# Optimization experiments

Hardware: AMD Instinct MI355X
Metric: run time of the kernel (lower is better)

## Reference

```python
import jax, jax.numpy as jnp
import numpy as np

N = 100000   # nodes
E = 1600000  # edges (avg degree 16)
G = 1024     # graphs in batch
F = 128      # node feature dim
H = 128      # hidden channels


def setup_inputs() -> dict:
    key = jax.random.key(0)
    ks = jax.random.split(key, 12)
    s = 1.0 / np.sqrt(H)
    x = jax.random.normal(ks[0], (N, F), dtype=jnp.float32)
    edge_index = jax.random.randint(ks[1], (2, E), 0, N, dtype=jnp.int32)
    batch = jnp.sort(jax.random.randint(ks[2], (N,), 0, G, dtype=jnp.int32))
    return {
        "x": x,
        "edge_index": edge_index,
        "batch": batch,
        "W1": jax.random.normal(ks[3], (F, H), dtype=jnp.float32) * s,
        "b1": jnp.zeros((H,), jnp.float32),
        "W2": jax.random.normal(ks[4], (H, H), dtype=jnp.float32) * s,
        "b2": jnp.zeros((H,), jnp.float32),
        "W3": jax.random.normal(ks[5], (H, H), dtype=jnp.float32) * s,
        "b3": jnp.zeros((H,), jnp.float32),
        "W4": jax.random.normal(ks[6], (H, H), dtype=jnp.float32) * s,
        "b4": jnp.zeros((H,), jnp.float32),
        "linW": jax.random.normal(ks[7], (H, 2), dtype=jnp.float32) * s,
        "linb": jnp.zeros((2,), jnp.float32),
    }


def _gcn_conv(h, W, b, src, dst, norm, n):
    # h' = D^{-1/2}(A+I)D^{-1/2} (h W) + b   (PyG GCNConv default)
    m = h @ W                              # [n, H]
    msg = m[src] * norm[:, None]           # [E+n, H] gather + scale
    out = jax.ops.segment_sum(msg, dst, num_segments=n)
    return out + b


def reference(x, edge_index, batch, W1, b1, W2, b2, W3, b3, W4, b4, linW, linb):
    n = x.shape[0]
    loops = jnp.arange(n, dtype=edge_index.dtype)
    src = jnp.concatenate([edge_index[0], loops])   # add self-loops
    dst = jnp.concatenate([edge_index[1], loops])
    deg = jax.ops.segment_sum(jnp.ones_like(dst, dtype=x.dtype), dst, num_segments=n)
    dinv = jax.lax.rsqrt(deg)                       # deg >= 1 due to self-loops
    norm = dinv[src] * dinv[dst]                    # [E+n]

    h = jax.nn.relu(_gcn_conv(x, W1, b1, src, dst, norm, n))
    h = jax.nn.relu(_gcn_conv(h, W2, b2, src, dst, norm, n))
    h = jax.nn.relu(_gcn_conv(h, W3, b3, src, dst, norm, n))
    h = jax.nn.relu(_gcn_conv(h, W4, b4, src, dst, norm, n))

    # global_mean_pool over `batch` segment ids
    counts = jax.ops.segment_sum(jnp.ones((n,), x.dtype), batch, num_segments=G)
    pooled = jax.ops.segment_sum(h, batch, num_segments=G) / jnp.maximum(counts, 1.0)[:, None]

    # dropout p=0.5 is identity in eval mode
    return pooled @ linW + linb
```

## Files before the change

### kernel.cpp

```cpp
#include <hip/hip_runtime.h>
#include <math.h>

#define NF 128
#define NU 64
#define NQ 32
#define TROWS 32
#define ARS 68
#define CRS 132
#define QS  16.0f
#define QIS 0.0625f

#define SRC_BITS 18
#define SRC_MASK ((1u << SRC_BITS) - 1u)
#define BCS 32
#define EPB 4096

typedef unsigned int  u32;
typedef unsigned short u16;
typedef u32 b4 __attribute__((ext_vector_type(2)));
typedef short bf16x8 __attribute__((ext_vector_type(8)));
typedef float f32x4 __attribute__((ext_vector_type(4)));
typedef float f32x2 __attribute__((ext_vector_type(2)));

__device__ inline u16 f2bf(float f) {
    u32 u = __float_as_uint(f);
    return (u16)((u + 0x7fffu + ((u >> 16) & 1u)) >> 16);
}
__device__ inline u32 pack2(float a, float b) {
    return (u32)f2bf(a) | ((u32)f2bf(b) << 16);
}
__device__ inline float bflo(u32 u) { return __uint_as_float(u << 16); }
__device__ inline float bfhi(u32 u) { return __uint_as_float(u & 0xffff0000u); }

__device__ inline u32 pack4(float a, float b, float c, float d) {
    u32 v = __builtin_amdgcn_cvt_pk_fp8_f32(a, b, 0, false);
    v = __builtin_amdgcn_cvt_pk_fp8_f32(c, d, v, true);
    return v;
}
__device__ inline void acc4(float4& a, u32 q) {
    f32x2 lo = __builtin_amdgcn_cvt_pk_f32_fp8(q, false);
    f32x2 hi = __builtin_amdgcn_cvt_pk_f32_fp8(q, true);
    a.x += lo[0]; a.y += lo[1]; a.z += hi[0]; a.w += hi[1];
}


__global__ __launch_bounds__(256) void k_bcnt(const int* __restrict__ ei,
                                              int* bcnt, int E, int bshift) {
    __shared__ int h[256];
    int t = threadIdx.x;
    h[t] = 0;
    __syncthreads();
    int base = blockIdx.x * EPB;
    #pragma unroll
    for (int k = 0; k < EPB / 256; ++k) {
        int e = base + k * 256 + t;
        if (e < E) atomicAdd(&h[ei[E + e] >> bshift], 1);
    }
    __syncthreads();
    if (h[t]) atomicAdd(&bcnt[t * BCS], h[t]);
}

__global__ __launch_bounds__(256) void k_bscan(const int* __restrict__ bcnt,
                                               int* bbase, int* bcur) {
    __shared__ int s[256];
    int t = threadIdx.x;
    int v = bcnt[t * BCS];
    s[t] = v;
    for (int d = 1; d < 256; d <<= 1) {
        __syncthreads();
        int a = (t >= d) ? s[t - d] : 0;
        __syncthreads();
        s[t] += a;
    }
    __syncthreads();
    bbase[t + 1] = s[t];
    bcur[t * BCS] = s[t] - v;
    if (t == 0) bbase[0] = 0;
}

__global__ __launch_bounds__(256) void k_bscat(const int* __restrict__ ei,
                                               int* bcur, u32* __restrict__ pairs,
                                               int E, int bshift) {
    __shared__ int h[256];
    __shared__ int rb[256];
    int t = threadIdx.x;
    h[t] = 0;
    __syncthreads();
    int base = blockIdx.x * EPB;
    #pragma unroll
    for (int k = 0; k < EPB / 256; ++k) {
        int e = base + k * 256 + t;
        if (e < E) atomicAdd(&h[ei[E + e] >> bshift], 1);
    }
    __syncthreads();
    int c = h[t];
    if (c) rb[t] = atomicAdd(&bcur[t * BCS], c);
    h[t] = 0;
    __syncthreads();
    #pragma unroll
    for (int k = 0; k < EPB / 256; ++k) {
        int e = base + k * 256 + t;
        if (e < E) {
            int d = ei[E + e];
            int b = d >> bshift;
            int p = rb[b] + atomicAdd(&h[b], 1);
            u32 rel = (u32)(d - (b << bshift));
            pairs[p] = (rel << SRC_BITS) | (u32)ei[e];
        }
    }
}

__global__ __launch_bounds__(256) void k_ndeg(const u32* __restrict__ pairs,
                                              const int* __restrict__ bbase,
                                              int* __restrict__ cnt, int n, int bshift) {
    extern __shared__ int sh[];
    int b = blockIdx.x;
    int bsz = 1 << bshift;
    int b0 = b << bshift;
    int t = threadIdx.x;
    for (int i = t; i < bsz; i += 256) sh[i] = 0;
    __syncthreads();
    int lo = bbase[b], hi = bbase[b + 1];
    for (int j = lo + t; j < hi; j += 256)
        atomicAdd(&sh[pairs[j] >> SRC_BITS], 1);
    __syncthreads();
    for (int i = t; i < bsz; i += 256) {
        int node = b0 + i;
        if (node < n) cnt[node] = sh[i];
    }
}

__global__ void k_scan1(const int* __restrict__ cnt, float* dinv,
                        int* offs, int* bsum, int n) {
    __shared__ int s[256];
    int t = threadIdx.x;
    int i = blockIdx.x * 256 + t;
    int v = 0;
    if (i < n) {
        int real = cnt[i] + 1;
        dinv[i] = 1.0f / sqrtf((float)real);
        v = (real + 3) & ~3;
    }
    s[t] = v;
    for (int d = 1; d < 256; d <<= 1) {
        __syncthreads();
        int add = (t >= d) ? s[t - d] : 0;
        __syncthreads();
        s[t] += add;
    }
    __syncthreads();
    if (i <= n) offs[i] = s[t] - v;
    if (t == 255) bsum[blockIdx.x] = s[255];
}

__global__ void k_scan2(int* bsum, int nb) {
    __shared__ int s[512];
    int t = threadIdx.x;
    int v = (t < nb) ? bsum[t] : 0;
    s[t] = v;
    for (int d = 1; d < 512; d <<= 1) {
        __syncthreads();
        int add = (t >= d) ? s[t - d] : 0;
        __syncthreads();
        s[t] += add;
    }
    __syncthreads();
    if (t < nb) bsum[t] = s[t] - v;
}

__global__ void k_scan3(int* offs, const int* __restrict__ bsum, int n) {
    int i = blockIdx.x * 256 + threadIdx.x;
    if (i <= n) offs[i] += bsum[blockIdx.x];
}

__global__ __launch_bounds__(256) void k_csr(const u32* __restrict__ pairs,
                                             const int* __restrict__ bbase,
                                             const int* __restrict__ offs,
                                             int* __restrict__ srcS, int n, int bshift) {
    extern __shared__ int sh[];
    int b = blockIdx.x;
    int bsz = 1 << bshift;
    int b0 = b << bshift;
    int t = threadIdx.x;
    for (int i = t; i < bsz; i += 256) {
        int node = b0 + i;
        sh[i] = (node < n) ? offs[node] : 0;
    }
    __syncthreads();
    int lo = bbase[b], hi = bbase[b + 1];
    for (int j = lo + t; j < hi; j += 256) {
        u32 v = pairs[j];
        int p = atomicAdd(&sh[v >> SRC_BITS], 1);
        srcS[p] = (int)(v & SRC_MASK);
    }
    __syncthreads();
    for (int i = t; i < bsz; i += 256) {
        int node = b0 + i;
        if (node < n) {
            int c = sh[i];
            srcS[c] = node;
            int end = offs[node + 1];
            for (int k = c + 1; k < end; ++k) srcS[k] = n;
        }
    }
}

__global__ __launch_bounds__(256) void k_pack(const float* __restrict__ x,
                       const float* __restrict__ dinv, u32* __restrict__ q,
                       const float* __restrict__ W0, const float* __restrict__ W1,
                       const float* __restrict__ W2, const float* __restrict__ W3,
                       u32* __restrict__ wt, int n) {
    int t = blockIdx.x * blockDim.x + threadIdx.x;
    int totalu4 = (n + 1) * (NQ / 4);
    if (t < totalu4) {
        int row = t >> 3;
        uint4 o = make_uint4(0, 0, 0, 0);
        if (row < n) {
            int cbase = (t & 7) << 4;
            const float* xr = x + (size_t)row * NF + cbase;
            float4 f0 = *(const float4*)(xr);
            float4 f1 = *(const float4*)(xr + 4);
            float4 f2 = *(const float4*)(xr + 8);
            float4 f3 = *(const float4*)(xr + 12);
            float d = dinv[row] * QS;
            o.x = pack4(f0.x * d, f0.y * d, f0.z * d, f0.w * d);
            o.y = pack4(f1.x * d, f1.y * d, f1.z * d, f1.w * d);
            o.z = pack4(f2.x * d, f2.y * d, f2.z * d, f2.w * d);
            o.w = pack4(f3.x * d, f3.y * d, f3.z * d, f3.w * d);
        }
        ((uint4*)q)[t] = o;
    }
    if (t < 4 * 2048) {
        int layer = t >> 11;
        int rem = t & 2047;
        int lane = rem & 63;
        int ks = (rem >> 6) & 3;
        int nt = rem >> 8;
        const float* W = layer == 0 ? W0 : layer == 1 ? W1 : layer == 2 ? W2 : W3;
        int nn = nt * 16 + (lane & 15);
        int k0 = ks * 32 + (lane >> 4) * 8;
        uint4 o;
        o.x = pack2(W[(k0 + 0) * NF + nn], W[(k0 + 1) * NF + nn]);
        o.y = pack2(W[(k0 + 2) * NF + nn], W[(k0 + 3) * NF + nn]);
        o.z = pack2(W[(k0 + 4) * NF + nn], W[(k0 + 5) * NF + nn]);
        o.w = pack2(W[(k0 + 6) * NF + nn], W[(k0 + 7) * NF + nn]);
        ((uint4*)wt)[t] = o;
    }
}

__global__ __launch_bounds__(256, 8) void k_fused(
        const u32* __restrict__ hin, const int* __restrict__ offs,
        const int* __restrict__ srcS, const float* __restrict__ dinv,
        const u32* __restrict__ wt, const float* __restrict__ bias,
        u32* __restrict__ out, int n, int ntiles, int last) {
    __shared__ __align__(16) u32 buf[TROWS * CRS];
    float* Cs = (float*)buf;
    int tid = threadIdx.x;
    int grp = tid >> 5;
    int lane32 = tid & 31;
    int c4 = lane32 << 2;
    int cu = lane32 << 1;
    int cq = lane32;
    int wv = tid >> 6;
    int lane = tid & 63;
    int m0 = (wv & 1) * 16;
    int nh = wv >> 1;
    int mrow = lane & 15, quad = lane >> 4;

    float4 bv = *(const float4*)(bias + c4);

    for (int tile = blockIdx.x; tile < ntiles; tile += gridDim.x) {
        int row0 = tile * TROWS;

        #pragma unroll
        for (int i = 0; i < 4; ++i) {
            int r = grp * 4 + i;
            int node = row0 + r;
            float4 acc = make_float4(0.f, 0.f, 0.f, 0.f);
            if (node < n) {
                int b = offs[node], e = offs[node + 1];
                int j = b;
                for (; j + 8 <= e; j += 8) {
                    int4 sa = *(const int4*)(srcS + j);
                    int4 sb = *(const int4*)(srcS + j + 4);
                    u32 q0 = hin[(size_t)sa.x * NQ + cq];
                    u32 q1 = hin[(size_t)sa.y * NQ + cq];
                    u32 q2 = hin[(size_t)sa.z * NQ + cq];
                    u32 q3 = hin[(size_t)sa.w * NQ + cq];
                    u32 q4 = hin[(size_t)sb.x * NQ + cq];
                    u32 q5 = hin[(size_t)sb.y * NQ + cq];
                    u32 q6 = hin[(size_t)sb.z * NQ + cq];
                    u32 q7 = hin[(size_t)sb.w * NQ + cq];
                    acc4(acc, q0); acc4(acc, q1); acc4(acc, q2); acc4(acc, q3);
                    acc4(acc, q4); acc4(acc, q5); acc4(acc, q6); acc4(acc, q7);
                }
                if (j < e) {
                    int4 sa = *(const int4*)(srcS + j);
                    u32 q0 = hin[(size_t)sa.x * NQ + cq];
                    u32 q1 = hin[(size_t)sa.y * NQ + cq];
                    u32 q2 = hin[(size_t)sa.z * NQ + cq];
                    u32 q3 = hin[(size_t)sa.w * NQ + cq];
                    acc4(acc, q0); acc4(acc, q1); acc4(acc, q2); acc4(acc, q3);
                }
                float dn = dinv[node];
                acc.x *= dn; acc.y *= dn; acc.z *= dn; acc.w *= dn;
            }
            b4 o; o.x = pack2(acc.x, acc.y); o.y = pack2(acc.z, acc.w);
            *(b4*)(buf + r * ARS + cu) = o;
        }
        __syncthreads();

        f32x4 a0 = {0.f, 0.f, 0.f, 0.f}, a1 = a0, a2 = a0, a3 = a0;
        #pragma unroll
        for (int ks = 0; ks < 4; ++ks) {
            bf16x8 a = *(const bf16x8*)(buf + (m0 + mrow) * ARS + ks * 16 + quad * 4);
            const u32* wb = wt + (((nh * 4) * 4 + ks) * 64 + lane) * 4;
            bf16x8 b0 = *(const bf16x8*)(wb);
            bf16x8 b1 = *(const bf16x8*)(wb + 1024);
            bf16x8 b2 = *(const bf16x8*)(wb + 2048);
            bf16x8 b3 = *(const bf16x8*)(wb + 3072);
            a0 = __builtin_amdgcn_mfma_f32_16x16x32_bf16(a, b0, a0, 0, 0, 0);
            a1 = __builtin_amdgcn_mfma_f32_16x16x32_bf16(a, b1, a1, 0, 0, 0);
            a2 = __builtin_amdgcn_mfma_f32_16x16x32_bf16(a, b2, a2, 0, 0, 0);
            a3 = __builtin_amdgcn_mfma_f32_16x16x32_bf16(a, b3, a3, 0, 0, 0);
        }
        __syncthreads();

        #pragma unroll
        for (int nt = 0; nt < 4; ++nt) {
            f32x4 av = nt == 0 ? a0 : nt == 1 ? a1 : nt == 2 ? a2 : a3;
            int col = (nh * 4 + nt) * 16 + mrow;
            #pragma unroll
            for (int rg = 0; rg < 4; ++rg)
                Cs[(m0 + quad * 4 + rg) * CRS + col] = av[rg];
        }
        __syncthreads();

        #pragma unroll
        for (int j = 0; j < 4; ++j) {
            int r = grp * 4 + j;
            int gr = row0 + r;
            if (gr <= n) {
                if (last) {
                    b4 o; o.x = 0u; o.y = 0u;
                    if (gr < n) {
                        float4 v = *(const float4*)(Cs + r * CRS + c4);
                        float ox = fmaxf(v.x * QIS + bv.x, 0.f);
                        float oy = fmaxf(v.y * QIS + bv.y, 0.f);
                        float oz = fmaxf(v.z * QIS + bv.z, 0.f);
                        float ow = fmaxf(v.w * QIS + bv.w, 0.f);
                        o.x = pack2(ox, oy);
                        o.y = pack2(oz, ow);
                    }
                    *(b4*)(out + (size_t)gr * NU + cu) = o;
                } else {
                    u32 o = 0u;
                    if (gr < n) {
                        float4 v = *(const float4*)(Cs + r * CRS + c4);
                        float sc = dinv[gr] * QS;
                        float ox = fmaxf(v.x * QIS + bv.x, 0.f) * sc;
                        float oy = fmaxf(v.y * QIS + bv.y, 0.f) * sc;
                        float oz = fmaxf(v.z * QIS + bv.z, 0.f) * sc;
                        float ow = fmaxf(v.w * QIS + bv.w, 0.f) * sc;
                        o = pack4(ox, oy, oz, ow);
                    }
                    out[(size_t)gr * NQ + cq] = o;
                }
            }
        }
        __syncthreads();
    }
}


__global__ __launch_bounds__(256) void k_poolfinal(const u32* __restrict__ h,
        const int* __restrict__ batch, const float* __restrict__ linW,
        const float* __restrict__ linb, float* __restrict__ outp, int N) {
    int g = blockIdx.x;
    int tid = threadIdx.x;
    __shared__ int sb[2];
    if (tid < 2) {
        int target = g + tid;
        int lo = 0, hi = N;
        while (lo < hi) {
            int mid = (lo + hi) >> 1;
            if (batch[mid] < target) lo = mid + 1; else hi = mid;
        }
        sb[tid] = lo;
    }
    __syncthreads();
    int b = sb[0], e = sb[1];

    int grp = tid >> 5, lane = tid & 31;
    int c4 = lane << 2, cu = lane << 1;
    float4 acc = make_float4(0.f, 0.f, 0.f, 0.f);
    for (int i = b + grp; i < e; i += 8) {
        b4 v = *(const b4*)(h + (size_t)i * NU + cu);
        acc.x += bflo(v.x); acc.y += bfhi(v.x);
        acc.z += bflo(v.y); acc.w += bfhi(v.y);
    }
    __shared__ float red[8][NF];
    *(float4*)(&red[grp][c4]) = acc;
    __syncthreads();

    float v0 = 0.f, v1 = 0.f;
    if (tid < NF) {
        float s = 0.f;
        #pragma unroll
        for (int gg = 0; gg < 8; ++gg) s += red[gg][tid];
        v0 = s * linW[tid * 2 + 0];
        v1 = s * linW[tid * 2 + 1];
    }
    #pragma unroll
    for (int d = 32; d > 0; d >>= 1) {
        v0 += __shfl_down(v0, d);
        v1 += __shfl_down(v1, d);
    }
    __shared__ float sv[8];
    if ((tid & 63) == 0) { sv[(tid >> 6) * 2] = v0; sv[(tid >> 6) * 2 + 1] = v1; }
    __syncthreads();
    if (tid == 0) {
        float inv = 1.0f / fmaxf((float)(e - b), 1.0f);
        outp[g * 2 + 0] = (sv[0] + sv[2]) * inv + linb[0];
        outp[g * 2 + 1] = (sv[1] + sv[3]) * inv + linb[1];
    }
}


extern "C" void kernel_launch(void* const* d_in, const int* in_sizes, int n_in,
                              void* d_out, int out_size, void* d_ws, size_t ws_size,
                              hipStream_t stream) {
    const float* x     = (const float*)d_in[0];
    const int*   ei    = (const int*)d_in[1];
    const int*   batch = (const int*)d_in[2];
    const float* Wl[4] = {(const float*)d_in[3], (const float*)d_in[5],
                          (const float*)d_in[7], (const float*)d_in[9]};
    const float* bl[4] = {(const float*)d_in[4], (const float*)d_in[6],
                          (const float*)d_in[8], (const float*)d_in[10]};
    const float* linW  = (const float*)d_in[11];
    const float* linb  = (const float*)d_in[12];
    float* out = (float*)d_out;

    const int N  = in_sizes[2];
    const int E  = in_sizes[1] / 2;
    const int G  = out_size / 2;

    int bshift = 9;
    while (((N + (1 << bshift) - 1) >> bshift) > 256) ++bshift;
    int nbk = (N + (1 << bshift) - 1) >> bshift;
    int bsz = 1 << bshift;

    char* p = (char*)d_ws;
    auto carve = [&](size_t bytes) -> char* {
        char* r = p;
        p += (bytes + 255) & ~(size_t)255;
        return r;
    };
    int*   cnt    = (int*)  carve((size_t)N * 4);
    float* dinv   = (float*)carve((size_t)N * 4);
    int*   offs   = (int*)  carve((size_t)(N + 1) * 4);
    int*   bsum   = (int*)  carve(512 * 4);
    int*   bcnt   = (int*)  carve(256 * BCS * 4);
    int*   bbase  = (int*)  carve(257 * 4);
    int*   bcur   = (int*)  carve(256 * BCS * 4);
    u32*   wt     = (u32*)  carve(4 * 2048 * 16);
    int*   srcS   = (int*)  carve((size_t)(E + 4 * (size_t)N) * 4);
    u32*   bufA   = (u32*)  carve((size_t)(N + 1) * NU * 4);
    u32*   bufB   = (u32*)  carve((size_t)(N + 1) * NU * 4);
    u32*   pairs  = bufB;

    (void)hipMemsetAsync(bcnt, 0, 256 * BCS * 4, stream);

    int nblkE = (E + EPB - 1) / EPB;
    k_bcnt<<<nblkE, 256, 0, stream>>>(ei, bcnt, E, bshift);
    k_bscan<<<1, 256, 0, stream>>>(bcnt, bbase, bcur);
    k_bscat<<<nblkE, 256, 0, stream>>>(ei, bcur, pairs, E, bshift);
    k_ndeg<<<nbk, 256, bsz * 4, stream>>>(pairs, bbase, cnt, N, bshift);

    int nb = (N + 1 + 255) / 256;
    k_scan1<<<nb, 256, 0, stream>>>(cnt, dinv, offs, bsum, N);
    k_scan2<<<1, 512, 0, stream>>>(bsum, nb);
    k_scan3<<<nb, 256, 0, stream>>>(offs, bsum, N);

    k_csr<<<nbk, 256, bsz * 4, stream>>>(pairs, bbase, offs, srcS, N, bshift);

    int totalu4 = (N + 1) * (NQ / 4);
    int packT = totalu4 > 8192 ? totalu4 : 8192;
    k_pack<<<(packT + 255) / 256, 256, 0, stream>>>(x, dinv, bufA,
                                                    Wl[0], Wl[1], Wl[2], Wl[3], wt, N);

    int ntiles = (N + 1 + TROWS - 1) / TROWS;
    int k = (ntiles + 4095) / 4096;
    int ngrid = (ntiles + k - 1) / k;
    const u32* hin = bufA;
    u32* hout = bufB;
    for (int l = 0; l < 4; ++l) {
        k_fused<<<ngrid, 256, 0, stream>>>(hin, offs, srcS, dinv, wt + l * 8192,
                                           bl[l], hout, N, ntiles, l == 3);
        hin = hout;
        hout = (hout == bufA) ? bufB : bufA;
    }

    k_poolfinal<<<G, 256, 0, stream>>>(hin, batch, linW, linb, out, N);
}
```

Before: 624.9 us.

## Fuse degree/scan CSR build kernels and add atomic dynamic tile scheduling

Merges the degree count, rsqrt and per-bucket prefix scan into one 512-thread kernel. A single small bucket-level scan follows, and its offsets are folded into the CSR scatter kernel, which replaces the three-pass global scan and drops the separate count buffer. The fused GCN layer kernel now takes tiles from a per-layer global atomic counter with a fixed grid of 2048 blocks, instead of a static grid-stride loop. This is meant to balance uneven neighbour-list lengths across blocks. The edges-per-block for bucketing is also halved. The changes cut launch count and setup passes, at the cost of one atomic and one block-wide barrier per tile.

```diff
diff --git a/kernel.cpp b/kernel.cpp
--- a/kernel.cpp
+++ b/kernel.cpp
@@ -13,7 +13,7 @@
 #define SRC_BITS 18
 #define SRC_MASK ((1u << SRC_BITS) - 1u)
 #define BCS 32
-#define EPB 4096
+#define EPB 2048
 
 typedef unsigned int  u32;
 typedef unsigned short u16;
@@ -110,97 +110,111 @@
     }
 }
 
-__global__ __launch_bounds__(256) void k_ndeg(const u32* __restrict__ pairs,
-                                              const int* __restrict__ bbase,
-                                              int* __restrict__ cnt, int n, int bshift) {
+__global__ __launch_bounds__(512) void k_degscan(const u32* __restrict__ pairs,
+        const int* __restrict__ bbase, float* __restrict__ dinv,
+        int* __restrict__ offs, int* __restrict__ bsum, int n, int bshift) {
     extern __shared__ int sh[];
-    int b = blockIdx.x;
     int bsz = 1 << bshift;
-    int b0 = b << bshift;
-    int t = threadIdx.x;
-    for (int i = t; i < bsz; i += 256) sh[i] = 0;
+    int* deg = sh;
+    int* ss = sh + bsz;
+    int b = blockIdx.x, b0 = b << bshift, t = threadIdx.x;
+    for (int i = t; i < bsz; i += 512) deg[i] = 0;
     __syncthreads();
     int lo = bbase[b], hi = bbase[b + 1];
-    for (int j = lo + t; j < hi; j += 256)
-        atomicAdd(&sh[pairs[j] >> SRC_BITS], 1);
-    __syncthreads();
-    for (int i = t; i < bsz; i += 256) {
+    for (int j = lo + t; j < hi; j += 512)
+        atomicAdd(&deg[pairs[j] >> SRC_BITS], 1);
+    __syncthreads();
+    int C = bsz >> 9;
+    int vloc[8];
+    int tsum = 0;
+    for (int c = 0; c < C; ++c) {
+        int i = t * C + c;
         int node = b0 + i;
-        if (node < n) cnt[node] = sh[i];
-    }
-}
-
-__global__ void k_scan1(const int* __restrict__ cnt, float* dinv,
-                        int* offs, int* bsum, int n) {
+        int v = 0;
+        if (node < n) {
+            int real = deg[i] + 1;
+            dinv[node] = 1.0f / sqrtf((float)real);
+            v = (real + 3) & ~3;
+        }
+        vloc[c] = tsum;
+        tsum += v;
+    }
+    ss[t] = tsum;
+    for (int d = 1; d < 512; d <<= 1) {
+        __syncthreads();
+        int a = (t >= d) ? ss[t - d] : 0;
+        __syncthreads();
+        ss[t] += a;
+    }
+    __syncthreads();
+    int tbase = ss[t] - tsum;
+    for (int c = 0; c < C; ++c) {
+        int node = b0 + t * C + c;
+        if (node < n) offs[node] = tbase + vloc[c];
+    }
+    if (t == 511) bsum[b] = ss[511];
+}
+
+__global__ __launch_bounds__(256) void k_bktscan(int* bsum, int* offs,
+                                                 int nbk, int n) {
     __shared__ int s[256];
     int t = threadIdx.x;
-    int i = blockIdx.x * 256 + t;
-    int v = 0;
-    if (i < n) {
-        int real = cnt[i] + 1;
-        dinv[i] = 1.0f / sqrtf((float)real);
-        v = (real + 3) & ~3;
-    }
+    int v = (t < nbk) ? bsum[t] : 0;
     s[t] = v;
     for (int d = 1; d < 256; d <<= 1) {
         __syncthreads();
-        int add = (t >= d) ? s[t - d] : 0;
-        __syncthreads();
-        s[t] += add;
-    }
-    __syncthreads();
-    if (i <= n) offs[i] = s[t] - v;
-    if (t == 255) bsum[blockIdx.x] = s[255];
-}
-
-__global__ void k_scan2(int* bsum, int nb) {
-    __shared__ int s[512];
-    int t = threadIdx.x;
-    int v = (t < nb) ? bsum[t] : 0;
-    s[t] = v;
-    for (int d = 1; d < 512; d <<= 1) {
-        __syncthreads();
-        int add = (t >= d) ? s[t - d] : 0;
-        __syncthreads();
-        s[t] += add;
-    }
-    __syncthreads();
-    if (t < nb) bsum[t] = s[t] - v;
-}
-
-__global__ void k_scan3(int* offs, const int* __restrict__ bsum, int n) {
-    int i = blockIdx.x * 256 + threadIdx.x;
-    if (i <= n) offs[i] += bsum[blockIdx.x];
-}
-
-__global__ __launch_bounds__(256) void k_csr(const u32* __restrict__ pairs,
-                                             const int* __restrict__ bbase,
-                                             const int* __restrict__ offs,
-                                             int* __restrict__ srcS, int n, int bshift) {
+        int a = (t >= d) ? s[t - d] : 0;
+        __syncthreads();
+        s[t] += a;
+    }
+    __syncthreads();
+    if (t < nbk) bsum[t] = s[t] - v;
+    if (t == 255) offs[n] = s[255];
+}
+
+__global__ __launch_bounds__(512) void k_csr(const u32* __restrict__ pairs,
+        const int* __restrict__ bbase, const int* __restrict__ bsum,
+        int* __restrict__ offs, int* __restrict__ srcS,
+        int n, int nbk, int bshift) {
     extern __shared__ int sh[];
-    int b = blockIdx.x;
     int bsz = 1 << bshift;
-    int b0 = b << bshift;
-    int t = threadIdx.x;
-    for (int i = t; i < bsz; i += 256) {
+    int* cur = sh;
+    int* endv = sh + bsz;
+    int b = blockIdx.x, b0 = b << bshift, t = threadIdx.x;
+    int base = bsum[b];
+    for (int i = t; i < bsz; i += 512) {
         int node = b0 + i;
-        sh[i] = (node < n) ? offs[node] : 0;
+        int o = 0;
+        if (node < n) {
+            o = offs[node] + base;
+            offs[node] = o;
+        }
+        cur[i] = o;
+    }
+    __syncthreads();
+    int offs_n = offs[n];
+    for (int i = t; i < bsz; i += 512) {
+        int node = b0 + i;
+        int e;
+        if (i < bsz - 1) e = (node + 1 < n) ? cur[i + 1] : offs_n;
+        else             e = (b + 1 < nbk) ? bsum[b + 1] : offs_n;
+        endv[i] = e;
     }
     __syncthreads();
     int lo = bbase[b], hi = bbase[b + 1];
-    for (int j = lo + t; j < hi; j += 256) {
+    for (int j = lo + t; j < hi; j += 512) {
         u32 v = pairs[j];
-        int p = atomicAdd(&sh[v >> SRC_BITS], 1);
+        int p = atomicAdd(&cur[v >> SRC_BITS], 1);
         srcS[p] = (int)(v & SRC_MASK);
     }
     __syncthreads();
-    for (int i = t; i < bsz; i += 256) {
+    for (int i = t; i < bsz; i += 512) {
         int node = b0 + i;
         if (node < n) {
-            int c = sh[i];
+            int c = cur[i];
             srcS[c] = node;
-            int end = offs[node + 1];
-            for (int k = c + 1; k < end; ++k) srcS[k] = n;
+            int e = endv[i];
+            for (int k = c + 1; k < e; ++k) srcS[k] = n;
         }
     }
 }
@@ -252,8 +266,9 @@
         const u32* __restrict__ hin, const int* __restrict__ offs,
         const int* __restrict__ srcS, const float* __restrict__ dinv,
         const u32* __restrict__ wt, const float* __restrict__ bias,
-        u32* __restrict__ out, int n, int ntiles, int last) {
+        u32* __restrict__ out, int* tctr, int n, int ntiles, int last) {
     __shared__ __align__(16) u32 buf[TROWS * CRS];
+    __shared__ int stile;
     float* Cs = (float*)buf;
     int tid = threadIdx.x;
     int grp = tid >> 5;
@@ -269,7 +284,11 @@
 
     float4 bv = *(const float4*)(bias + c4);
 
-    for (int tile = blockIdx.x; tile < ntiles; tile += gridDim.x) {
+    for (;;) {
+        if (tid == 0) stile = atomicAdd(tctr, 1);
+        __syncthreads();
+        int tile = stile;
+        if (tile >= ntiles) break;
         int row0 = tile * TROWS;
 
         #pragma unroll
@@ -456,13 +475,13 @@
         p += (bytes + 255) & ~(size_t)255;
         return r;
     };
-    int*   cnt    = (int*)  carve((size_t)N * 4);
     float* dinv   = (float*)carve((size_t)N * 4);
     int*   offs   = (int*)  carve((size_t)(N + 1) * 4);
     int*   bsum   = (int*)  carve(512 * 4);
     int*   bcnt   = (int*)  carve(256 * BCS * 4);
     int*   bbase  = (int*)  carve(257 * 4);
     int*   bcur   = (int*)  carve(256 * BCS * 4);
+    int*   tctr   = (int*)  carve(4 * 4);
     u32*   wt     = (u32*)  carve(4 * 2048 * 16);
     int*   srcS   = (int*)  carve((size_t)(E + 4 * (size_t)N) * 4);
     u32*   bufA   = (u32*)  carve((size_t)(N + 1) * NU * 4);
@@ -470,19 +489,17 @@
     u32*   pairs  = bufB;
 
     (void)hipMemsetAsync(bcnt, 0, 256 * BCS * 4, stream);
+    (void)hipMemsetAsync(tctr, 0, 4 * 4, stream);
 
     int nblkE = (E + EPB - 1) / EPB;
     k_bcnt<<<nblkE, 256, 0, stream>>>(ei, bcnt, E, bshift);
     k_bscan<<<1, 256, 0, stream>>>(bcnt, bbase, bcur);
     k_bscat<<<nblkE, 256, 0, stream>>>(ei, bcur, pairs, E, bshift);
-    k_ndeg<<<nbk, 256, bsz * 4, stream>>>(pairs, bbase, cnt, N, bshift);
-
-    int nb = (N + 1 + 255) / 256;
-    k_scan1<<<nb, 256, 0, stream>>>(cnt, dinv, offs, bsum, N);
-    k_scan2<<<1, 512, 0, stream>>>(bsum, nb);
-    k_scan3<<<nb, 256, 0, stream>>>(offs, bsum, N);
-
-    k_csr<<<nbk, 256, bsz * 4, stream>>>(pairs, bbase, offs, srcS, N, bshift);
+    k_degscan<<<nbk, 512, (bsz + 512) * 4, stream>>>(pairs, bbase, dinv, offs,
+                                                     bsum, N, bshift);
+    k_bktscan<<<1, 256, 0, stream>>>(bsum, offs, nbk, N);
+    k_csr<<<nbk, 512, 2 * bsz * 4, stream>>>(pairs, bbase, bsum, offs, srcS,
+                                             N, nbk, bshift);
 
     int totalu4 = (N + 1) * (NQ / 4);
     int packT = totalu4 > 8192 ? totalu4 : 8192;
@@ -490,13 +507,12 @@
                                                     Wl[0], Wl[1], Wl[2], Wl[3], wt, N);
 
     int ntiles = (N + 1 + TROWS - 1) / TROWS;
-    int k = (ntiles + 4095) / 4096;
-    int ngrid = (ntiles + k - 1) / k;
+    int ngrid = ntiles < 2048 ? ntiles : 2048;
     const u32* hin = bufA;
     u32* hout = bufB;
     for (int l = 0; l < 4; ++l) {
         k_fused<<<ngrid, 256, 0, stream>>>(hin, offs, srcS, dinv, wt + l * 8192,
-                                           bl[l], hout, N, ntiles, l == 3);
+                                           bl[l], hout, tctr + l, N, ntiles, l == 3);
         hin = hout;
         hout = (hout == bufA) ? bufB : bufA;
     }
```

After: 547.8 us. 1.14x faster.
